# Kernel tuning notes

Hardware: AMD Instinct MI355X
Metric: run time of the kernel (lower is better)

## Reference

```python
import jax, jax.numpy as jnp
import numpy as np

B, NJ, NM = 64, 30, 20
N = NJ * NM          # 600 operation nodes per FJSP instance
IN_DIM, H = 2, 128


def _bn(h):
    # torch BatchNorm1d in training mode, gamma=1/beta=0 (module init), stats over all nodes
    m = h.mean(axis=(0, 1))
    v = h.var(axis=(0, 1))
    return (h - m) / jnp.sqrt(v + 1e-5)


def setup_inputs() -> dict:
    key = jax.random.key(0)
    ks = jax.random.split(key, 20)
    x = jax.random.normal(ks[0], (B, N, IN_DIM), jnp.float32)
    graph_pool = jnp.full((B, N), 1.0 / N, jnp.float32)   # average graph pooling weights
    padded_nei = jnp.zeros((1,), jnp.int32)               # unused (sum pooling path)
    adj = (jax.random.uniform(ks[1], (B, N, N)) < 0.01).astype(jnp.float32)
    adj = jnp.minimum(adj + jnp.eye(N, dtype=jnp.float32)[None], 1.0)  # self-loops
    candidate = jax.random.randint(ks[2], (B, NJ), 0, N)
    a_index = jax.random.randint(ks[3], (B,), 0, NJ)
    mask = jax.random.uniform(ks[4], (B, NJ)) < 0.2
    mask = mask.at[jnp.arange(B), a_index].set(False)     # chosen action never masked
    mask_mch = jax.random.uniform(ks[5], (B, N, NM)) < 0.3
    dur = jax.random.uniform(ks[6], (B, N, NM), dtype=jnp.float32)
    old_action = jax.random.randint(ks[7], (B,), 0, N)
    mch_pool = jax.random.normal(ks[8], (B, H), jnp.float32)

    def w(k, i, o):
        return jax.random.normal(k, (i, o), jnp.float32) * (1.0 / np.sqrt(i))

    z = lambda n: jnp.zeros((n,), jnp.float32)            # biases init to 0 in module
    return dict(
        x=x, graph_pool=graph_pool, padded_nei=padded_nei, adj=adj,
        candidate=candidate, mask=mask, mask_mch=mask_mch, dur=dur,
        a_index=a_index, old_action=old_action, mch_pool=mch_pool,
        W1_0=w(ks[9], IN_DIM, H), b1_0=z(H), W2_0=w(ks[10], H, H), b2_0=z(H),
        W1_1=w(ks[11], H, H), b1_1=z(H), W2_1=w(ks[12], H, H), b2_1=z(H),
        Wa1=w(ks[13], 3 * H, H), ba1=z(H), Wa2=w(ks[14], H, H), ba2=z(H),
        Wa3=w(ks[15], H, 1), ba3=z(1),
        Wc1=w(ks[16], H, H), bc1=z(H), Wc2=w(ks[17], H, 1), bc2=z(1),
    )


def reference(x, graph_pool, padded_nei, adj, candidate, mask, mask_mch, dur,
              a_index, old_action, mch_pool,
              W1_0, b1_0, W2_0, b2_0, W1_1, b1_1, W2_1, b2_1,
              Wa1, ba1, Wa2, ba2, Wa3, ba3, Wc1, bc1, Wc2, bc2):
    # --- GIN encoder: num_layers-1 = 2 message-passing layers, sum pooling ---
    h = x
    for (W1, b1, W2, b2) in ((W1_0, b1_0, W2_0, b2_0), (W1_1, b1_1, W2_1, b2_1)):
        pooled = jnp.einsum('bnm,bmd->bnd', adj, h)         # neighbor sum (adj has self-loops)
        h1 = jax.nn.relu(_bn(pooled @ W1 + b1))             # MLP hidden (BN inside MLP)
        h = jax.nn.relu(_bn(h1 @ W2 + b2))                  # layer BN + relu
    h_nodes = h                                             # [B, N, H]
    h_pooled = jnp.einsum('bn,bnd->bd', graph_pool, h_nodes)  # [B, H]

    # --- gather candidate features, concat pooled contexts ---
    cand_feat = jnp.take_along_axis(h_nodes, candidate[:, :, None], axis=1)  # [B, NJ, H]
    concat = jnp.concatenate([
        cand_feat,
        jnp.broadcast_to(h_pooled[:, None, :], cand_feat.shape),
        jnp.broadcast_to(mch_pool[:, None, :], cand_feat.shape)], axis=-1)   # [B, NJ, 3H]

    # --- MLPActor(3 layers, tanh) ---
    a = jnp.tanh(concat @ Wa1 + ba1)
    a = jnp.tanh(a @ Wa2 + ba2)
    scores = (a @ Wa3 + ba3).squeeze(-1) * 10.0             # [B, NJ]
    scores = jnp.where(mask, -jnp.inf, scores)
    logpi = jax.nn.log_softmax(scores, axis=1)
    pi = jnp.exp(logpi)
    log_a = jnp.take_along_axis(logpi, a_index[:, None], axis=1)[:, 0]
    entropy = -jnp.sum(jnp.where(pi > 0, pi * logpi, 0.0), axis=1)

    # --- gather action-dependent tensors (detached in torch) ---
    b_idx = jnp.arange(B)
    action_node = dur[b_idx, old_action]                    # [B, NM]
    action_feature = h_nodes[b_idx, old_action]             # [B, H]
    mask_mch_action = mask_mch[b_idx, old_action][:, None, :]  # [B, 1, NM]

    # --- MLPCritic(2 layers, tanh) ---
    v = jnp.tanh(h_pooled @ Wc1 + bc1) @ Wc2 + bc2          # [B, 1]

    sg = jax.lax.stop_gradient
    return (entropy, v, log_a, sg(action_node), sg(action_feature),
            mask_mch_action, sg(h_pooled))
```

## Files before the change

### kernel.cpp

```cpp
#include <hip/hip_runtime.h>
#include <hip/hip_bf16.h>

#define BB 64
#define NJ 30
#define NM 20
#define NN 600
#define HH 128
#define NROWS (BB*NN)
#define CAP 48

typedef __attribute__((ext_vector_type(8))) short short8;
typedef __attribute__((ext_vector_type(4))) float f32x4;

#define STATS_B   0
#define HPOOL_B   4096
#define FLAGS_B   36864
#define ZERO_B    36880
#define WTB_B     37120
#define SCORES_B  135424
#define NBRCNT_B  143104
#define NBRIDX_B  296704
#define POOLED0_B 7669504
#define T1_B      7976704
#define P1_B      27637504

#define OUT_ENT   0
#define OUT_V     64
#define OUT_LOGA  128
#define OUT_ANODE 192
#define OUT_AFEAT 1472
#define OUT_MMCH  9664
#define OUT_HPOOL 10944

__device__ __forceinline__ bool mask_at(const void* p, int layout, long i) {
    if (layout == 2) return ((const float*)p)[i] != 0.f;
    if (layout == 1) return ((const unsigned char*)p)[i] != 0;
    return ((const int*)p)[i] != 0;
}

__device__ __forceinline__ short bf16rne(float f) {
    unsigned u = __float_as_uint(f);
    return (short)((u + 0x7fffu + ((u >> 16) & 1u)) >> 16);
}
__device__ __forceinline__ float bf2f(unsigned h) {
    return __uint_as_float(h << 16);
}
__device__ __forceinline__ unsigned packbf(float a, float b) {
    return ((unsigned)(unsigned short)bf16rne(a)) |
           (((unsigned)(unsigned short)bf16rne(b)) << 16);
}

__global__ __launch_bounds__(256) void k_sparse(const float* __restrict__ adj,
                                                const float* __restrict__ x,
                                                int* __restrict__ nbr_cnt,
                                                int* __restrict__ nbr_idx,
                                                float* __restrict__ pooled0,
                                                const void* mask_p, const void* maskmch_p,
                                                int* flags,
                                                const float* __restrict__ Wa,
                                                const float* __restrict__ Wb,
                                                const float* __restrict__ Wc,
                                                unsigned short* __restrict__ wT) {
    int bid = blockIdx.x;
    int tid = threadIdx.x;
    if (bid < 289) {
        if (bid >= 97) {
            int bid2 = bid - 97;
            int mat = bid2 >> 6;
            int idx = ((bid2 & 63) << 8) + tid;
            const float* W = mat == 0 ? Wa : (mat == 1 ? Wb : Wc);
            int k = idx >> 7, c = idx & 127;
            wT[mat * 16384 + c * HH + k] = (unsigned short)bf16rne(W[idx]);
        } else {
            unsigned agg = 0;
            int which;
            if (bid == 0) {
                which = 0;
                const unsigned* p = (const unsigned*)mask_p;
                unsigned w0 = (tid < 480) ? p[tid] : 0u;
                unsigned w1 = (tid + 256 < 480) ? p[tid + 256] : 0u;
                agg = w0 | w1;
            } else {
                which = 1;
                const unsigned* p = (const unsigned*)maskmch_p + (size_t)(bid - 1) * 200;
                agg = (tid < 200) ? p[tid] : 0u;
            }
            int f = 0;
            if (((agg >> 24) & 0xffu) == 0x3fu) f |= 1;
            if ((((agg >> 8) & 0xffu) == 1u) || (((agg >> 16) & 0xffu) == 1u) ||
                (((agg >> 24) & 0xffu) == 1u)) f |= 2;
#pragma unroll
            for (int off = 1; off < 64; off <<= 1) f |= __shfl_xor(f, off);
            if ((tid & 63) == 0 && f) atomicOr(&flags[which], f);
        }
    }

    int wrow = bid * 4 + (tid >> 6);
    int lane = tid & 63;
    int b = wrow / NN;
    const float4* arow = (const float4*)(adj + (size_t)wrow * NN);
    int* irow = nbr_idx + (size_t)wrow * CAP;
    const float* xb = x + (size_t)b * NN * 2;
    float4 vv[3];
    vv[0] = arow[lane];
    vv[1] = arow[64 + lane];
    vv[2] = (128 + lane < 150) ? arow[128 + lane] : make_float4(0.f, 0.f, 0.f, 0.f);
    unsigned long long below = (1ull << lane) - 1ull;
    int cnt = 0;
    float p0 = 0.f, p1 = 0.f;
#pragma unroll
    for (int it = 0; it < 3; ++it) {
        float4 v = vv[it];
        int col0 = it * 256 + lane * 4;
#pragma unroll
        for (int j = 0; j < 4; ++j) {
            float a = (j == 0) ? v.x : (j == 1) ? v.y : (j == 2) ? v.z : v.w;
            bool m = a != 0.f;
            unsigned long long bal = __ballot(m);
            if (m) {
                int pos = cnt + (int)__popcll(bal & below);
                if (pos < CAP) irow[pos] = col0 + j;
                float2 xv = *(const float2*)&xb[(col0 + j) * 2];
                p0 += xv.x; p1 += xv.y;
            }
            cnt += (int)__popcll(bal);
        }
    }
#pragma unroll
    for (int off = 1; off < 64; off <<= 1) {
        p0 += __shfl_xor(p0, off);
        p1 += __shfl_xor(p1, off);
    }
    if (lane == 0) {
        nbr_cnt[wrow] = cnt < CAP ? cnt : CAP;
        pooled0[(size_t)wrow * 2]     = p0;
        pooled0[(size_t)wrow * 2 + 1] = p1;
    }
}

__global__ __launch_bounds__(256) void k_p0stats(const float* __restrict__ pooled0,
                                                 float* __restrict__ out5) {
    __shared__ float red[4][5];
    int i = blockIdx.x * 256 + threadIdx.x;
    float p0 = pooled0[(size_t)i * 2], p1 = pooled0[(size_t)i * 2 + 1];
    float v[5] = {p0, p1, p0 * p0, p1 * p1, p0 * p1};
#pragma unroll
    for (int j = 0; j < 5; ++j)
#pragma unroll
        for (int off = 1; off < 64; off <<= 1) v[j] += __shfl_xor(v[j], off);
    int lane = threadIdx.x & 63, w = threadIdx.x >> 6;
    if (lane == 0)
#pragma unroll
        for (int j = 0; j < 5; ++j) red[w][j] = v[j];
    __syncthreads();
    if (threadIdx.x == 0)
#pragma unroll
        for (int j = 0; j < 5; ++j)
            atomicAdd(&out5[j], red[0][j] + red[1][j] + red[2][j] + red[3][j]);
}

template<int MODE>
__global__ __launch_bounds__(256) void k_stage(const void* __restrict__ t_in_v,
                                               const float* __restrict__ pooled0,
                                               const float* __restrict__ W1,
                                               const unsigned short* __restrict__ wT,
                                               const float* __restrict__ stats_in,
                                               unsigned short* __restrict__ t_out,
                                               float* __restrict__ stats_out) {
    __shared__ float sm_mean[HH], sm_inv[HH];
    __shared__ float smS[4][32], smQ[4][32];
    int tid = threadIdx.x;
    if (MODE == 0 && tid < HH) {
        float S0 = stats_in[0], S1 = stats_in[1], Q0 = stats_in[2], Q1 = stats_in[3], P01 = stats_in[4];
        float w0 = W1[tid], w1 = W1[HH + tid];
        float m = (S0 * w0 + S1 * w1) * (1.f / NROWS);
        float eq = (Q0 * w0 * w0 + Q1 * w1 * w1 + 2.f * P01 * w0 * w1) * (1.f / NROWS);
        sm_mean[tid] = m;
        sm_inv[tid] = 1.f / sqrtf(eq - m * m + 1e-5f);
    }
    if (MODE == 1 && tid < HH) {
        float s = stats_in[tid], q = stats_in[HH + tid];
        float m = s * (1.f / NROWS);
        sm_mean[tid] = m;
        sm_inv[tid] = 1.f / sqrtf(q * (1.f / NROWS) - m * m + 1e-5f);
    }
    if (MODE != 2) __syncthreads();

    const unsigned short* tin = (const unsigned short*)t_in_v;
    int lane = tid & 63, wave = tid >> 6;
    int r16 = lane & 15, kg = lane >> 4;
    int rowbase = (blockIdx.x >> 2) * 64 + wave * 16;
    int colq = blockIdx.x & 3;

    f32x4 acc[2];
#pragma unroll
    for (int t = 0; t < 2; ++t)
#pragma unroll
        for (int i = 0; i < 4; ++i) acc[t][i] = 0.f;

    float p0 = 0.f, p1 = 0.f;
    if (MODE == 0) {
        p0 = pooled0[(size_t)(rowbase + r16) * 2];
        p1 = pooled0[(size_t)(rowbase + r16) * 2 + 1];
    }

#pragma unroll
    for (int ks = 0; ks < 4; ++ks) {
        int kb = ks * 32 + kg * 8;
        short8 afr;
        if (MODE == 2) {
            afr = *(const short8*)&tin[(size_t)(rowbase + r16) * HH + kb];
        } else {
            float av[8];
            if (MODE == 0) {
                float4 wa0 = *(const float4*)&W1[kb];
                float4 wa1 = *(const float4*)&W1[kb + 4];
                float4 wb0 = *(const float4*)&W1[HH + kb];
                float4 wb1 = *(const float4*)&W1[HH + kb + 4];
                av[0] = p0 * wa0.x + p1 * wb0.x; av[1] = p0 * wa0.y + p1 * wb0.y;
                av[2] = p0 * wa0.z + p1 * wb0.z; av[3] = p0 * wa0.w + p1 * wb0.w;
                av[4] = p0 * wa1.x + p1 * wb1.x; av[5] = p0 * wa1.y + p1 * wb1.y;
                av[6] = p0 * wa1.z + p1 * wb1.z; av[7] = p0 * wa1.w + p1 * wb1.w;
            } else {
                short8 raw = *(const short8*)&tin[(size_t)(rowbase + r16) * HH + kb];
#pragma unroll
                for (int j = 0; j < 8; ++j) av[j] = bf2f((unsigned short)raw[j]);
            }
            float4 m0 = *(const float4*)&sm_mean[kb];
            float4 m1 = *(const float4*)&sm_mean[kb + 4];
            float4 i0 = *(const float4*)&sm_inv[kb];
            float4 i1 = *(const float4*)&sm_inv[kb + 4];
            av[0] = fmaxf((av[0] - m0.x) * i0.x, 0.f);
            av[1] = fmaxf((av[1] - m0.y) * i0.y, 0.f);
            av[2] = fmaxf((av[2] - m0.z) * i0.z, 0.f);
            av[3] = fmaxf((av[3] - m0.w) * i0.w, 0.f);
            av[4] = fmaxf((av[4] - m1.x) * i1.x, 0.f);
            av[5] = fmaxf((av[5] - m1.y) * i1.y, 0.f);
            av[6] = fmaxf((av[6] - m1.z) * i1.z, 0.f);
            av[7] = fmaxf((av[7] - m1.w) * i1.w, 0.f);
#pragma unroll
            for (int j = 0; j < 8; ++j) afr[j] = bf16rne(av[j]);
        }
#pragma unroll
        for (int t = 0; t < 2; ++t) {
            short8 bfr = *(const short8*)&wT[(size_t)((colq * 2 + t) * 16 + r16) * HH + kb];
            acc[t] = __builtin_amdgcn_mfma_f32_16x16x32_bf16(afr, bfr, acc[t], 0, 0, 0);
        }
    }

#pragma unroll
    for (int t = 0; t < 2; ++t) {
        int lc = t * 16 + r16;
        int col = colq * 32 + lc;
        float s = 0.f, q = 0.f;
#pragma unroll
        for (int i = 0; i < 4; ++i) {
            float v = acc[t][i];
            t_out[(size_t)(rowbase + kg * 4 + i) * HH + col] = (unsigned short)bf16rne(v);
            s += v; q += v * v;
        }
        s += __shfl_xor(s, 16); q += __shfl_xor(q, 16);
        s += __shfl_xor(s, 32); q += __shfl_xor(q, 32);
        if (kg == 0) { smS[wave][lc] = s; smQ[wave][lc] = q; }
    }
    __syncthreads();
    if (tid < 32) {
        int col = colq * 32 + tid;
        atomicAdd(&stats_out[col],      smS[0][tid] + smS[1][tid] + smS[2][tid] + smS[3][tid]);
        atomicAdd(&stats_out[HH + col], smQ[0][tid] + smQ[1][tid] + smQ[2][tid] + smQ[3][tid]);
    }
}

__global__ __launch_bounds__(256) void k_pool1(const unsigned short* __restrict__ t1,
                                               const int* __restrict__ nbr_cnt,
                                               const int* __restrict__ nbr_idx,
                                               const float* __restrict__ stats1,
                                               unsigned short* __restrict__ pooled1) {
    __shared__ float sm_mean[HH], sm_inv[HH];
    int tid = threadIdx.x;
    if (tid < HH) {
        float s = stats1[tid], q = stats1[HH + tid];
        float m = s * (1.f / NROWS);
        sm_mean[tid] = m;
        sm_inv[tid] = 1.f / sqrtf(q * (1.f / NROWS) - m * m + 1e-5f);
    }
    __syncthreads();
    int c4 = tid & 31, rl = tid >> 5;
    int row = blockIdx.x * 8 + rl;
    int b = row / NN;
    float4 mm = *(const float4*)&sm_mean[c4 * 4];
    float4 iv = *(const float4*)&sm_inv[c4 * 4];
    int cnt = nbr_cnt[row];
    const int* ir = nbr_idx + (size_t)row * CAP;
    const unsigned short* tb = t1 + (size_t)b * NN * HH;
    float a0 = 0.f, a1 = 0.f, a2 = 0.f, a3 = 0.f;
    int i = 0;
    for (; i + 1 < cnt; i += 2) {
        int m0 = ir[i], m1 = ir[i + 1];
        uint2 w0 = *(const uint2*)&tb[(size_t)m0 * HH + c4 * 4];
        uint2 w1 = *(const uint2*)&tb[(size_t)m1 * HH + c4 * 4];
        a0 += fmaxf((bf2f(w0.x & 0xffffu) - mm.x) * iv.x, 0.f)
            + fmaxf((bf2f(w1.x & 0xffffu) - mm.x) * iv.x, 0.f);
        a1 += fmaxf((bf2f(w0.x >> 16)     - mm.y) * iv.y, 0.f)
            + fmaxf((bf2f(w1.x >> 16)     - mm.y) * iv.y, 0.f);
        a2 += fmaxf((bf2f(w0.y & 0xffffu) - mm.z) * iv.z, 0.f)
            + fmaxf((bf2f(w1.y & 0xffffu) - mm.z) * iv.z, 0.f);
        a3 += fmaxf((bf2f(w0.y >> 16)     - mm.w) * iv.w, 0.f)
            + fmaxf((bf2f(w1.y >> 16)     - mm.w) * iv.w, 0.f);
    }
    if (i < cnt) {
        int m0 = ir[i];
        uint2 w0 = *(const uint2*)&tb[(size_t)m0 * HH + c4 * 4];
        a0 += fmaxf((bf2f(w0.x & 0xffffu) - mm.x) * iv.x, 0.f);
        a1 += fmaxf((bf2f(w0.x >> 16)     - mm.y) * iv.y, 0.f);
        a2 += fmaxf((bf2f(w0.y & 0xffffu) - mm.z) * iv.z, 0.f);
        a3 += fmaxf((bf2f(w0.y >> 16)     - mm.w) * iv.w, 0.f);
    }
    uint2 o;
    o.x = packbf(a0, a1);
    o.y = packbf(a2, a3);
    *(uint2*)&pooled1[(size_t)row * HH + c4 * 4] = o;
}

__global__ __launch_bounds__(256) void k_hpool(const unsigned short* __restrict__ t3,
                                               const float* __restrict__ gp,
                                               const float* __restrict__ stats3,
                                               float* __restrict__ hpool) {
    __shared__ float sm_mean[HH], sm_inv[HH];
    __shared__ float red[8][HH];
    int tid = threadIdx.x;
    if (tid < HH) {
        float s = stats3[tid], q = stats3[HH + tid];
        float m = s * (1.f / NROWS);
        sm_mean[tid] = m;
        sm_inv[tid] = 1.f / sqrtf(q * (1.f / NROWS) - m * m + 1e-5f);
    }
    __syncthreads();
    int b = blockIdx.x >> 3, chunk = blockIdx.x & 7;
    int c4 = tid & 31, rl = tid >> 5;
    float4 mm = *(const float4*)&sm_mean[c4 * 4];
    float4 iv = *(const float4*)&sm_inv[c4 * 4];
    float a0 = 0.f, a1 = 0.f, a2 = 0.f, a3 = 0.f;
    int nend = chunk * 75 + 75;
    for (int n = chunk * 75 + rl; n < nend; n += 8) {
        float w = gp[b * NN + n];
        uint2 t = *(const uint2*)&t3[((size_t)b * NN + n) * HH + c4 * 4];
        a0 += w * fmaxf((bf2f(t.x & 0xffffu) - mm.x) * iv.x, 0.f);
        a1 += w * fmaxf((bf2f(t.x >> 16)     - mm.y) * iv.y, 0.f);
        a2 += w * fmaxf((bf2f(t.y & 0xffffu) - mm.z) * iv.z, 0.f);
        a3 += w * fmaxf((bf2f(t.y >> 16)     - mm.w) * iv.w, 0.f);
    }
    *(float4*)&red[rl][c4 * 4] = make_float4(a0, a1, a2, a3);
    __syncthreads();
    if (tid < HH) {
        float s = 0.f;
#pragma unroll
        for (int g = 0; g < 8; ++g) s += red[g][tid];
        atomicAdd(&hpool[b * HH + tid], s);
    }
}

__global__ __launch_bounds__(256) void k_actor(const unsigned short* __restrict__ t3,
                                               const int* __restrict__ cand,
                                               const float* __restrict__ hpool,
                                               const float* __restrict__ mch,
                                               const float* __restrict__ stats3,
                                               const float* __restrict__ Wa1,
                                               const float* __restrict__ ba1,
                                               const float* __restrict__ Wa2,
                                               const float* __restrict__ ba2,
                                               const float* __restrict__ Wa3,
                                               const float* __restrict__ ba3,
                                               float* __restrict__ scores) {
    __shared__ float sh_c[8 * 384];
    __shared__ float sh_a1[8 * HH];
    __shared__ float sred[8][HH];
    int tid = threadIdx.x;
    int rbase = blockIdx.x * 8;
    int c = tid & 127, slot = tid >> 7;

    float mean_c, inv_c;
    {
        float s = stats3[c], q = stats3[HH + c];
        float m = s * (1.f / NROWS);
        mean_c = m;
        inv_c = 1.f / sqrtf(q * (1.f / NROWS) - m * m + 1e-5f);
    }
#pragma unroll
    for (int rr = 0; rr < 4; ++rr) {
        int r = slot * 4 + rr;
        int row = rbase + r;
        int b = row / NJ;
        int cd = cand[row];
        float v = bf2f(t3[((size_t)b * NN + cd) * HH + c]);
        sh_c[r * 384 + c]       = fmaxf((v - mean_c) * inv_c, 0.f);
        sh_c[r * 384 + 128 + c] = hpool[b * HH + c];
        sh_c[r * 384 + 256 + c] = mch[b * HH + c];
    }
    __syncthreads();

    float acc[4] = {0.f, 0.f, 0.f, 0.f};
    for (int k = 0; k < 384; ++k) {
        float w = Wa1[(size_t)k * HH + c];
#pragma unroll
        for (int rr = 0; rr < 4; ++rr)
            acc[rr] += sh_c[(slot * 4 + rr) * 384 + k] * w;
    }
    float bb = ba1[c];
#pragma unroll
    for (int rr = 0; rr < 4; ++rr)
        sh_a1[(slot * 4 + rr) * HH + c] = tanhf(acc[rr] + bb);
    __syncthreads();

    float acc2[4] = {0.f, 0.f, 0.f, 0.f};
    for (int k = 0; k < HH; ++k) {
        float w = Wa2[(size_t)k * HH + c];
#pragma unroll
        for (int rr = 0; rr < 4; ++rr)
            acc2[rr] += sh_a1[(slot * 4 + rr) * HH + k] * w;
    }
    float w3 = Wa3[c], bb2 = ba2[c];
#pragma unroll
    for (int rr = 0; rr < 4; ++rr)
        sred[slot * 4 + rr][c] = tanhf(acc2[rr] + bb2) * w3;
    __syncthreads();
    int r = tid >> 5, l32 = tid & 31;
    float v = sred[r][l32] + sred[r][l32 + 32] + sred[r][l32 + 64] + sred[r][l32 + 96];
    v += __shfl_xor(v, 1); v += __shfl_xor(v, 2); v += __shfl_xor(v, 4);
    v += __shfl_xor(v, 8); v += __shfl_xor(v, 16);
    if (l32 == 0) scores[rbase + r] = 10.f * (v + ba3[0]);
}

__global__ __launch_bounds__(128) void k_final(const unsigned short* __restrict__ t3,
                                               const float* __restrict__ stats3,
                                               const float* __restrict__ hpool,
                                               const float* __restrict__ scores,
                                               const void* __restrict__ mask_p,
                                               const void* __restrict__ maskmch_p,
                                               const int* __restrict__ flags,
                                               const float* __restrict__ dur,
                                               const int* __restrict__ a_index,
                                               const int* __restrict__ old_action,
                                               const float* __restrict__ Wc1,
                                               const float* __restrict__ bc1,
                                               const float* __restrict__ Wc2,
                                               const float* __restrict__ bc2,
                                               float* __restrict__ out) {
    __shared__ float sm_mean[HH], sm_inv[HH], sh_hp[HH], sh_red[HH];
    __shared__ float sh_s[32], sh_lp[32];
    __shared__ int sh_m[32];
    int b = blockIdx.x, t = threadIdx.x;
    {
        float s = stats3[t], q = stats3[HH + t];
        float m = s * (1.f / NROWS);
        sm_mean[t] = m;
        sm_inv[t] = 1.f / sqrtf(q * (1.f / NROWS) - m * m + 1e-5f);
    }
    sh_hp[t] = hpool[b * HH + t];
    __syncthreads();

    float acc = bc1[t];
    for (int k = 0; k < HH; ++k) acc += sh_hp[k] * Wc1[k * HH + t];
    sh_red[t] = tanhf(acc) * Wc2[t];
    __syncthreads();
    for (int st = 64; st > 0; st >>= 1) {
        if (t < st) sh_red[t] += sh_red[t + st];
        __syncthreads();
    }
    if (t == 0) out[OUT_V + b] = sh_red[0] + bc2[0];

    int fA = flags[0], fB = flags[1];
    int layA = (fA & 1) ? 2 : ((fA & 2) ? 1 : 0);
    int layB = (fB & 1) ? 2 : ((fB & 2) ? 1 : 0);
    if (t < NJ) {
        sh_s[t] = scores[b * NJ + t];
        sh_m[t] = mask_at(mask_p, layA, (long)b * NJ + t) ? 1 : 0;
    }
    __syncthreads();
    if (t == 0) {
        float mx = -1e30f;
        for (int j = 0; j < NJ; ++j)
            if (!sh_m[j] && sh_s[j] > mx) mx = sh_s[j];
        float sum = 0.f;
        for (int j = 0; j < NJ; ++j)
            if (!sh_m[j]) sum += expf(sh_s[j] - mx);
        float lse = mx + logf(sum);
        float ent = 0.f;
        for (int j = 0; j < NJ; ++j) {
            if (!sh_m[j]) {
                float lp = sh_s[j] - lse;
                sh_lp[j] = lp;
                float pi = expf(lp);
                if (pi > 0.f) ent -= pi * lp;
            }
        }
        out[OUT_ENT + b] = ent;
        out[OUT_LOGA + b] = sh_lp[a_index[b]];
    }

    int old = old_action[b];
    if (t < NM) {
        out[OUT_ANODE + b * NM + t] = dur[((size_t)b * NN + old) * NM + t];
        out[OUT_MMCH + b * NM + t] =
            mask_at(maskmch_p, layB, ((size_t)b * NN + old) * NM + t) ? 1.f : 0.f;
    }
    {
        float v = bf2f(t3[((size_t)b * NN + old) * HH + t]);
        out[OUT_AFEAT + b * HH + t] = fmaxf((v - sm_mean[t]) * sm_inv[t], 0.f);
        out[OUT_HPOOL + b * HH + t] = sh_hp[t];
    }
}

extern "C" void kernel_launch(void* const* d_in, const int* in_sizes, int n_in,
                              void* d_out, int out_size, void* d_ws, size_t ws_size,
                              hipStream_t stream) {
    (void)in_sizes; (void)n_in; (void)out_size; (void)ws_size;
    const float* x         = (const float*)d_in[0];
    const float* gp        = (const float*)d_in[1];
    const float* adj       = (const float*)d_in[3];
    const int*   cand      = (const int*)d_in[4];
    const void*  mask_p    = d_in[5];
    const void*  maskmch_p = d_in[6];
    const float* dur       = (const float*)d_in[7];
    const int*   a_index   = (const int*)d_in[8];
    const int*   old_act   = (const int*)d_in[9];
    const float* mch_pool  = (const float*)d_in[10];
    const float* W1_0 = (const float*)d_in[11];
    const float* W2_0 = (const float*)d_in[13];
    const float* W1_1 = (const float*)d_in[15];
    const float* W2_1 = (const float*)d_in[17];
    const float* Wa1  = (const float*)d_in[19];
    const float* ba1  = (const float*)d_in[20];
    const float* Wa2  = (const float*)d_in[21];
    const float* ba2  = (const float*)d_in[22];
    const float* Wa3  = (const float*)d_in[23];
    const float* ba3  = (const float*)d_in[24];
    const float* Wc1  = (const float*)d_in[25];
    const float* bc1  = (const float*)d_in[26];
    const float* Wc2  = (const float*)d_in[27];
    const float* bc2  = (const float*)d_in[28];

    char* ws = (char*)d_ws;
    float* stats   = (float*)(ws + STATS_B);
    float* hpool   = (float*)(ws + HPOOL_B);
    int*   flags   = (int*)(ws + FLAGS_B);
    unsigned short* wtb = (unsigned short*)(ws + WTB_B);
    float* scores  = (float*)(ws + SCORES_B);
    int*   nbr_cnt = (int*)(ws + NBRCNT_B);
    int*   nbr_idx = (int*)(ws + NBRIDX_B);
    float* pooled0 = (float*)(ws + POOLED0_B);
    unsigned short* t1_16 = (unsigned short*)(ws + T1_B);
    unsigned short* p1_16 = (unsigned short*)(ws + P1_B);
    float* out     = (float*)d_out;

    hipMemsetAsync(ws, 0, ZERO_B, stream);
    k_sparse<<<NROWS / 4, 256, 0, stream>>>(adj, x, nbr_cnt, nbr_idx, pooled0,
                                            mask_p, maskmch_p, flags, W2_0, W1_1, W2_1, wtb);
    k_p0stats<<<NROWS / 256, 256, 0, stream>>>(pooled0, stats);
    k_stage<0><<<2400, 256, 0, stream>>>(nullptr, pooled0, W1_0, wtb, stats, t1_16, stats + 256);
    k_pool1<<<NROWS / 8, 256, 0, stream>>>(t1_16, nbr_cnt, nbr_idx, stats + 256, p1_16);
    k_stage<2><<<2400, 256, 0, stream>>>(p1_16, nullptr, nullptr, wtb + 16384, stats, t1_16, stats + 512);
    k_stage<1><<<2400, 256, 0, stream>>>(t1_16, nullptr, nullptr, wtb + 32768, stats + 512,
                                         p1_16, stats + 768);
    k_hpool<<<BB * 8, 256, 0, stream>>>(p1_16, gp, stats + 768, hpool);
    k_actor<<<240, 256, 0, stream>>>(p1_16, cand, hpool, mch_pool, stats + 768,
                                     Wa1, ba1, Wa2, ba2, Wa3, ba3, scores);
    k_final<<<BB, 128, 0, stream>>>(p1_16, stats + 768, hpool, scores, mask_p, maskmch_p, flags,
                                    dur, a_index, old_act, Wc1, bc1, Wc2, bc2, out);
}
```

Before: 348.9 us.

## Replace sparse neighbor-list pooling with dense bf16 MFMA adjacency matmul

Drops the compacted neighbor-index lists and instead converts the adjacency matrix to padded bf16 while computing the layer-0 pooled input as a dense dot product. The layer-1 neighbor pooling becomes a dense per-graph adjacency × hidden matmul on MFMA, with normalized ReLU activations staged transposed in LDS. This removes the CAP=48 truncation and the irregular gathers, at the cost of dense O(N^2) work on a roughly 1%-dense matrix, an extra bf16 adjacency buffer, and bf16 rounding of adjacency and activations. The k_sparse launch also changes to 8 rows per block.

```diff
diff --git a/kernel.cpp b/kernel.cpp
--- a/kernel.cpp
+++ b/kernel.cpp
@@ -7,7 +7,7 @@
 #define NN 600
 #define HH 128
 #define NROWS (BB*NN)
-#define CAP 48
+#define KP 608
 
 typedef __attribute__((ext_vector_type(8))) short short8;
 typedef __attribute__((ext_vector_type(4))) float f32x4;
@@ -18,11 +18,10 @@
 #define ZERO_B    36880
 #define WTB_B     37120
 #define SCORES_B  135424
-#define NBRCNT_B  143104
-#define NBRIDX_B  296704
 #define POOLED0_B 7669504
 #define T1_B      7976704
 #define P1_B      27637504
+#define ADJB_B    50331648
 
 #define OUT_ENT   0
 #define OUT_V     64
@@ -52,9 +51,8 @@
 
 __global__ __launch_bounds__(256) void k_sparse(const float* __restrict__ adj,
                                                 const float* __restrict__ x,
-                                                int* __restrict__ nbr_cnt,
-                                                int* __restrict__ nbr_idx,
                                                 float* __restrict__ pooled0,
+                                                unsigned short* __restrict__ adjb,
                                                 const void* mask_p, const void* maskmch_p,
                                                 int* flags,
                                                 const float* __restrict__ Wa,
@@ -95,46 +93,65 @@
         }
     }
 
-    int wrow = bid * 4 + (tid >> 6);
-    int lane = tid & 63;
-    int b = wrow / NN;
-    const float4* arow = (const float4*)(adj + (size_t)wrow * NN);
-    int* irow = nbr_idx + (size_t)wrow * CAP;
-    const float* xb = x + (size_t)b * NN * 2;
-    float4 vv[3];
-    vv[0] = arow[lane];
-    vv[1] = arow[64 + lane];
-    vv[2] = (128 + lane < 150) ? arow[128 + lane] : make_float4(0.f, 0.f, 0.f, 0.f);
-    unsigned long long below = (1ull << lane) - 1ull;
-    int cnt = 0;
-    float p0 = 0.f, p1 = 0.f;
-#pragma unroll
-    for (int it = 0; it < 3; ++it) {
-        float4 v = vv[it];
-        int col0 = it * 256 + lane * 4;
-#pragma unroll
-        for (int j = 0; j < 4; ++j) {
-            float a = (j == 0) ? v.x : (j == 1) ? v.y : (j == 2) ? v.z : v.w;
-            bool m = a != 0.f;
-            unsigned long long bal = __ballot(m);
-            if (m) {
-                int pos = cnt + (int)__popcll(bal & below);
-                if (pos < CAP) irow[pos] = col0 + j;
-                float2 xv = *(const float2*)&xb[(col0 + j) * 2];
-                p0 += xv.x; p1 += xv.y;
-            }
-            cnt += (int)__popcll(bal);
-        }
-    }
+    int wave = tid >> 6, lane = tid & 63;
+    int wr0 = bid * 8 + wave * 2;
+    int wr1 = wr0 + 1;
+    int b0 = wr0 / NN;
+    const float4* ar0 = (const float4*)(adj + (size_t)wr0 * NN);
+    const float4* ar1 = (const float4*)(adj + (size_t)wr1 * NN);
+    const float4 Z = make_float4(0.f, 0.f, 0.f, 0.f);
+    float4 va[3], vb[3];
+    va[0] = ar0[lane];
+    va[1] = ar0[64 + lane];
+    va[2] = (lane < 22) ? ar0[128 + lane] : Z;
+    vb[0] = ar1[lane];
+    vb[1] = ar1[64 + lane];
+    vb[2] = (lane < 22) ? ar1[128 + lane] : Z;
+
+    const float4* x0 = (const float4*)(x + (size_t)b0 * NN * 2);
+    float4 xl0[2], xl1[2], xl2[2];
+    xl0[0] = x0[lane * 2];        xl0[1] = x0[lane * 2 + 1];
+    xl1[0] = x0[128 + lane * 2];  xl1[1] = x0[128 + lane * 2 + 1];
+    if (lane < 22) { xl2[0] = x0[256 + lane * 2]; xl2[1] = x0[256 + lane * 2 + 1]; }
+    else           { xl2[0] = Z;  xl2[1] = Z; }
+
+    float p0a, p1a, p0b, p1b;
+    p0a = va[0].x * xl0[0].x + va[0].y * xl0[0].z + va[0].z * xl0[1].x + va[0].w * xl0[1].z
+        + va[1].x * xl1[0].x + va[1].y * xl1[0].z + va[1].z * xl1[1].x + va[1].w * xl1[1].z
+        + va[2].x * xl2[0].x + va[2].y * xl2[0].z + va[2].z * xl2[1].x + va[2].w * xl2[1].z;
+    p1a = va[0].x * xl0[0].y + va[0].y * xl0[0].w + va[0].z * xl0[1].y + va[0].w * xl0[1].w
+        + va[1].x * xl1[0].y + va[1].y * xl1[0].w + va[1].z * xl1[1].y + va[1].w * xl1[1].w
+        + va[2].x * xl2[0].y + va[2].y * xl2[0].w + va[2].z * xl2[1].y + va[2].w * xl2[1].w;
+    p0b = vb[0].x * xl0[0].x + vb[0].y * xl0[0].z + vb[0].z * xl0[1].x + vb[0].w * xl0[1].z
+        + vb[1].x * xl1[0].x + vb[1].y * xl1[0].z + vb[1].z * xl1[1].x + vb[1].w * xl1[1].z
+        + vb[2].x * xl2[0].x + vb[2].y * xl2[0].z + vb[2].z * xl2[1].x + vb[2].w * xl2[1].z;
+    p1b = vb[0].x * xl0[0].y + vb[0].y * xl0[0].w + vb[0].z * xl0[1].y + vb[0].w * xl0[1].w
+        + vb[1].x * xl1[0].y + vb[1].y * xl1[0].w + vb[1].z * xl1[1].y + vb[1].w * xl1[1].w
+        + vb[2].x * xl2[0].y + vb[2].y * xl2[0].w + vb[2].z * xl2[1].y + vb[2].w * xl2[1].w;
+
+    unsigned short* r0o = adjb + (size_t)wr0 * KP;
+    unsigned short* r1o = adjb + (size_t)wr1 * KP;
+    *(uint2*)&r0o[lane * 4]       = make_uint2(packbf(va[0].x, va[0].y), packbf(va[0].z, va[0].w));
+    *(uint2*)&r0o[256 + lane * 4] = make_uint2(packbf(va[1].x, va[1].y), packbf(va[1].z, va[1].w));
+    if (lane < 24)
+        *(uint2*)&r0o[512 + lane * 4] = make_uint2(packbf(va[2].x, va[2].y), packbf(va[2].z, va[2].w));
+    *(uint2*)&r1o[lane * 4]       = make_uint2(packbf(vb[0].x, vb[0].y), packbf(vb[0].z, vb[0].w));
+    *(uint2*)&r1o[256 + lane * 4] = make_uint2(packbf(vb[1].x, vb[1].y), packbf(vb[1].z, vb[1].w));
+    if (lane < 24)
+        *(uint2*)&r1o[512 + lane * 4] = make_uint2(packbf(vb[2].x, vb[2].y), packbf(vb[2].z, vb[2].w));
+
 #pragma unroll
     for (int off = 1; off < 64; off <<= 1) {
-        p0 += __shfl_xor(p0, off);
-        p1 += __shfl_xor(p1, off);
+        p0a += __shfl_xor(p0a, off);
+        p1a += __shfl_xor(p1a, off);
+        p0b += __shfl_xor(p0b, off);
+        p1b += __shfl_xor(p1b, off);
     }
     if (lane == 0) {
-        nbr_cnt[wrow] = cnt < CAP ? cnt : CAP;
-        pooled0[(size_t)wrow * 2]     = p0;
-        pooled0[(size_t)wrow * 2 + 1] = p1;
+        pooled0[(size_t)wr0 * 2]     = p0a;
+        pooled0[(size_t)wr0 * 2 + 1] = p1a;
+        pooled0[(size_t)wr1 * 2]     = p0b;
+        pooled0[(size_t)wr1 * 2 + 1] = p1b;
     }
 }
 
@@ -271,12 +288,12 @@
     }
 }
 
-__global__ __launch_bounds__(256) void k_pool1(const unsigned short* __restrict__ t1,
-                                               const int* __restrict__ nbr_cnt,
-                                               const int* __restrict__ nbr_idx,
+__global__ __launch_bounds__(256) void k_poolm(const unsigned short* __restrict__ t1,
+                                               const unsigned short* __restrict__ adjb,
                                                const float* __restrict__ stats1,
                                                unsigned short* __restrict__ pooled1) {
     __shared__ float sm_mean[HH], sm_inv[HH];
+    __shared__ unsigned short hT[HH * 40];
     int tid = threadIdx.x;
     if (tid < HH) {
         float s = stats1[tid], q = stats1[HH + tid];
@@ -285,41 +302,57 @@
         sm_inv[tid] = 1.f / sqrtf(q * (1.f / NROWS) - m * m + 1e-5f);
     }
     __syncthreads();
-    int c4 = tid & 31, rl = tid >> 5;
-    int row = blockIdx.x * 8 + rl;
-    int b = row / NN;
-    float4 mm = *(const float4*)&sm_mean[c4 * 4];
-    float4 iv = *(const float4*)&sm_inv[c4 * 4];
-    int cnt = nbr_cnt[row];
-    const int* ir = nbr_idx + (size_t)row * CAP;
+
+    int b = blockIdx.x / 10, mblk = blockIdx.x % 10;
+    int lane = tid & 63, wave = tid >> 6;
+    int r16 = lane & 15, kg = lane >> 4;
+    int rowbase = mblk * 64 + wave * 16;
+    int rowA = rowbase + r16; if (rowA > 599) rowA = 599;
+    const unsigned short* Abase = adjb + ((size_t)b * NN + rowA) * KP;
     const unsigned short* tb = t1 + (size_t)b * NN * HH;
-    float a0 = 0.f, a1 = 0.f, a2 = 0.f, a3 = 0.f;
-    int i = 0;
-    for (; i + 1 < cnt; i += 2) {
-        int m0 = ir[i], m1 = ir[i + 1];
-        uint2 w0 = *(const uint2*)&tb[(size_t)m0 * HH + c4 * 4];
-        uint2 w1 = *(const uint2*)&tb[(size_t)m1 * HH + c4 * 4];
-        a0 += fmaxf((bf2f(w0.x & 0xffffu) - mm.x) * iv.x, 0.f)
-            + fmaxf((bf2f(w1.x & 0xffffu) - mm.x) * iv.x, 0.f);
-        a1 += fmaxf((bf2f(w0.x >> 16)     - mm.y) * iv.y, 0.f)
-            + fmaxf((bf2f(w1.x >> 16)     - mm.y) * iv.y, 0.f);
-        a2 += fmaxf((bf2f(w0.y & 0xffffu) - mm.z) * iv.z, 0.f)
-            + fmaxf((bf2f(w1.y & 0xffffu) - mm.z) * iv.z, 0.f);
-        a3 += fmaxf((bf2f(w0.y >> 16)     - mm.w) * iv.w, 0.f)
-            + fmaxf((bf2f(w1.y >> 16)     - mm.w) * iv.w, 0.f);
-    }
-    if (i < cnt) {
-        int m0 = ir[i];
-        uint2 w0 = *(const uint2*)&tb[(size_t)m0 * HH + c4 * 4];
-        a0 += fmaxf((bf2f(w0.x & 0xffffu) - mm.x) * iv.x, 0.f);
-        a1 += fmaxf((bf2f(w0.x >> 16)     - mm.y) * iv.y, 0.f);
-        a2 += fmaxf((bf2f(w0.y & 0xffffu) - mm.z) * iv.z, 0.f);
-        a3 += fmaxf((bf2f(w0.y >> 16)     - mm.w) * iv.w, 0.f);
-    }
-    uint2 o;
-    o.x = packbf(a0, a1);
-    o.y = packbf(a2, a3);
-    *(uint2*)&pooled1[(size_t)row * HH + c4 * 4] = o;
+
+    int mg = tid >> 3, cg = tid & 7;
+
+    f32x4 acc[8];
+#pragma unroll
+    for (int t = 0; t < 8; ++t)
+#pragma unroll
+        for (int i = 0; i < 4; ++i) acc[t][i] = 0.f;
+
+    for (int kk = 0; kk < 19; ++kk) {
+        int m = kk * 32 + mg; if (m > 599) m = 599;
+        const unsigned short* trow = &tb[(size_t)m * HH];
+#pragma unroll
+        for (int p = 0; p < 2; ++p) {
+            int c0 = cg * 8 + p * 64;
+            short8 raw = *(const short8*)&trow[c0];
+#pragma unroll
+            for (int j = 0; j < 8; ++j) {
+                int c = c0 + j;
+                float v = fmaxf((bf2f((unsigned short)raw[j]) - sm_mean[c]) * sm_inv[c], 0.f);
+                hT[c * 40 + mg] = (unsigned short)bf16rne(v);
+            }
+        }
+        __syncthreads();
+        short8 afr = *(const short8*)&Abase[kk * 32 + kg * 8];
+#pragma unroll
+        for (int t = 0; t < 8; ++t) {
+            short8 bfr = *(const short8*)&hT[(t * 16 + r16) * 40 + kg * 8];
+            acc[t] = __builtin_amdgcn_mfma_f32_16x16x32_bf16(afr, bfr, acc[t], 0, 0, 0);
+        }
+        __syncthreads();
+    }
+
+#pragma unroll
+    for (int t = 0; t < 8; ++t) {
+        int col = t * 16 + r16;
+#pragma unroll
+        for (int i = 0; i < 4; ++i) {
+            int row = rowbase + kg * 4 + i;
+            if (row < NN)
+                pooled1[((size_t)b * NN + row) * HH + col] = (unsigned short)bf16rne(acc[t][i]);
+        }
+    }
 }
 
 __global__ __launch_bounds__(256) void k_hpool(const unsigned short* __restrict__ t3,
@@ -544,22 +577,22 @@
     float* stats   = (float*)(ws + STATS_B);
     float* hpool   = (float*)(ws + HPOOL_B);
     int*   flags   = (int*)(ws + FLAGS_B);
-    unsigned short* wtb = (unsigned short*)(ws + WTB_B);
+    unsigned short* wtb  = (unsigned short*)(ws + WTB_B);
     float* scores  = (float*)(ws + SCORES_B);
-    int*   nbr_cnt = (int*)(ws + NBRCNT_B);
-    int*   nbr_idx = (int*)(ws + NBRIDX_B);
     float* pooled0 = (float*)(ws + POOLED0_B);
     unsigned short* t1_16 = (unsigned short*)(ws + T1_B);
     unsigned short* p1_16 = (unsigned short*)(ws + P1_B);
+    unsigned short* adjb  = (unsigned short*)(ws + ADJB_B);
     float* out     = (float*)d_out;
 
     hipMemsetAsync(ws, 0, ZERO_B, stream);
-    k_sparse<<<NROWS / 4, 256, 0, stream>>>(adj, x, nbr_cnt, nbr_idx, pooled0,
+    k_sparse<<<NROWS / 8, 256, 0, stream>>>(adj, x, pooled0, adjb,
                                             mask_p, maskmch_p, flags, W2_0, W1_1, W2_1, wtb);
     k_p0stats<<<NROWS / 256, 256, 0, stream>>>(pooled0, stats);
     k_stage<0><<<2400, 256, 0, stream>>>(nullptr, pooled0, W1_0, wtb, stats, t1_16, stats + 256);
-    k_pool1<<<NROWS / 8, 256, 0, stream>>>(t1_16, nbr_cnt, nbr_idx, stats + 256, p1_16);
-    k_stage<2><<<2400, 256, 0, stream>>>(p1_16, nullptr, nullptr, wtb + 16384, stats, t1_16, stats + 512);
+    k_poolm<<<BB * 10, 256, 0, stream>>>(t1_16, adjb, stats + 256, p1_16);
+    k_stage<2><<<2400, 256, 0, stream>>>(p1_16, nullptr, nullptr, wtb + 16384, nullptr,
+                                         t1_16, stats + 512);
     k_stage<1><<<2400, 256, 0, stream>>>(t1_16, nullptr, nullptr, wtb + 32768, stats + 512,
                                          p1_16, stats + 768);
     k_hpool<<<BB * 8, 256, 0, stream>>>(p1_16, gp, stats + 768, hpool);
```

New measurement: 381.1 us. 9.2% more time.
